# Optimization experiments

Hardware: AMD Instinct MI355X
Metric: run time of the kernel (lower is better)

## Reference

```python
import jax, jax.numpy as jnp
import numpy as np

B, D, INNER, OUT = 8192, 256, 64, 256


def setup_inputs() -> dict:
    key = jax.random.key(0)
    ks = jax.random.split(key, 10)
    s = 0.1
    return {
        "x": jax.random.normal(ks[0], (B, D), dtype=jnp.float32),
        # per-feature inner MLPs: Linear(1, inner) -> ReLU -> Linear(inner, 1)
        "w1": jax.random.normal(ks[1], (D, INNER), dtype=jnp.float32) * s,
        "b1": jax.random.normal(ks[2], (D, INNER), dtype=jnp.float32) * s,
        "w2": jax.random.normal(ks[3], (D, INNER), dtype=jnp.float32) * s,
        "b2": jax.random.normal(ks[4], (D,), dtype=jnp.float32) * s,
        # outer MLP: Linear(D, inner) -> ReLU -> Linear(inner, out)
        "wo1": jax.random.normal(ks[5], (INNER, D), dtype=jnp.float32) * s,
        "bo1": jax.random.normal(ks[6], (INNER,), dtype=jnp.float32) * s,
        "wo2": jax.random.normal(ks[7], (OUT, INNER), dtype=jnp.float32) * s,
        "bo2": jax.random.normal(ks[8], (OUT,), dtype=jnp.float32) * s,
    }


def reference(x, w1, b1, w2, b2, wo1, bo1, wo2, bo2):
    # Vectorized per-feature tiny MLPs: h[b,d,i] = relu(x[b,d]*w1[d,i] + b1[d,i])
    h = jax.nn.relu(x[:, :, None] * w1[None, :, :] + b1[None, :, :])  # [B, D, INNER]
    inner = jnp.einsum('bdi,di->bd', h, w2) + b2[None, :]             # [B, D]
    # Outer MLP
    g = jax.nn.relu(inner @ wo1.T + bo1)                              # [B, INNER]
    return g @ wo2.T + bo2                                            # [B, OUT]
```

## Files before the change

### kernel.cpp

```cpp
#include <hip/hip_runtime.h>
#include <hip/hip_bf16.h>


#define B_TOT 8192
#define D_DIM 256
#define I_DIM 64
#define O_DIM 256
#define RB 16
#define NT 512

typedef __hip_bfloat16 bf16;
using short8 = __attribute__((ext_vector_type(8))) short;
using f32x4  = __attribute__((ext_vector_type(4))) float;


__global__ __launch_bounds__(256)
void kal_prep(const float* __restrict__ w1, const float* __restrict__ b1,
              const float* __restrict__ w2, const float* __restrict__ wo1,
              const float* __restrict__ wo2, float4* __restrict__ ws) {
    int idx = blockIdx.x * 256 + threadIdx.x;
    if (idx < 16384) {
        int i = idx >> 8;
        int d = idx & 255;
        ws[idx] = make_float4(w1[d * I_DIM + i], b1[d * I_DIM + i],
                              w2[d * I_DIM + i], 0.0f);
    } else if (idx < 32768) {
        int r  = idx - 16384;
        int kc = r >> 11;
        int rem = r & 2047;
        int j  = rem >> 5;
        int kk = rem & 31;
        bf16* pbB = (bf16*)(ws + 16384);
        pbB[r] = __float2bfloat16(wo1[j * D_DIM + kc * 32 + kk]);
    } else if (idx < 49152) {
        int r  = idx - 32768;
        int kc = r >> 13;
        int rem = r & 8191;
        int o  = rem >> 5;
        int kk = rem & 31;
        bf16* pcB = (bf16*)(ws + 16384) + 16384;
        pcB[r] = __float2bfloat16(wo2[o * I_DIM + kc * 32 + kk]);
    }
}

__global__ __launch_bounds__(NT)
void kal_main(const float* __restrict__ x,  const float* __restrict__ b2,
              const float* __restrict__ bo1, const float* __restrict__ bo2,
              const float4* __restrict__ ws, float* __restrict__ out) {
    const float4* pa  = ws;
    const bf16*   pbB = (const bf16*)(ws + 16384);
    const bf16*   pcB = pbB + 16384;

    __shared__ bf16 inner_bf[RB][264];
    __shared__ bf16 g_bf[RB][72];

    const int t    = threadIdx.x;
    const int row0 = blockIdx.x * RB;

    {
        const int d    = t & 255;
        const int half = t >> 8;
        float xv[8], acc[8];
        const float b2v = b2[d];
        #pragma unroll
        for (int b = 0; b < 8; ++b) {
            xv[b]  = x[(row0 + half * 8 + b) * D_DIM + d];
            acc[b] = b2v;
        }
        #pragma unroll 4
        for (int i = 0; i < I_DIM; ++i) {
            const float4 w = pa[i * D_DIM + d];
            #pragma unroll
            for (int b = 0; b < 8; ++b) {
                float h = fmaf(xv[b], w.x, w.y);
                h = fmaxf(h, 0.0f);
                acc[b] = fmaf(h, w.z, acc[b]);
            }
        }
        #pragma unroll
        for (int b = 0; b < 8; ++b)
            inner_bf[half * 8 + b][d] = __float2bfloat16(acc[b]);
    }
    __syncthreads();

    const int lane = t & 63;
    const int wave = t >> 6;
    const int col  = lane & 15;
    const int quad = lane >> 4;

    if (wave < 4) {
        const int j0 = wave * 16;
        f32x4 acc = {0.f, 0.f, 0.f, 0.f};
        #pragma unroll
        for (int kc = 0; kc < 8; ++kc) {
            short8 af = *(const short8*)&inner_bf[col][kc * 32 + quad * 8];
            short8 bfr = *(const short8*)&pbB[(kc * 64 + j0 + col) * 32 + quad * 8];
            acc = __builtin_amdgcn_mfma_f32_16x16x32_bf16(af, bfr, acc, 0, 0, 0);
        }
        const float bo1v = bo1[j0 + col];
        #pragma unroll
        for (int r = 0; r < 4; ++r) {
            const int row = quad * 4 + r;
            g_bf[row][j0 + col] = __float2bfloat16(fmaxf(acc[r] + bo1v, 0.0f));
        }
    }
    __syncthreads();

    #pragma unroll
    for (int tile = 0; tile < 2; ++tile) {
        const int o0 = wave * 16 + tile * 128;
        f32x4 acc = {0.f, 0.f, 0.f, 0.f};
        #pragma unroll
        for (int kc = 0; kc < 2; ++kc) {
            short8 af = *(const short8*)&g_bf[col][kc * 32 + quad * 8];
            short8 bfr = *(const short8*)&pcB[(kc * 256 + o0 + col) * 32 + quad * 8];
            acc = __builtin_amdgcn_mfma_f32_16x16x32_bf16(af, bfr, acc, 0, 0, 0);
        }
        const float bo2v = bo2[o0 + col];
        #pragma unroll
        for (int r = 0; r < 4; ++r)
            out[(row0 + quad * 4 + r) * O_DIM + o0 + col] = acc[r] + bo2v;
    }
}

extern "C" void kernel_launch(void* const* d_in, const int* in_sizes, int n_in,
                              void* d_out, int out_size, void* d_ws, size_t ws_size,
                              hipStream_t stream) {
    const float* x   = (const float*)d_in[0];
    const float* w1  = (const float*)d_in[1];
    const float* b1  = (const float*)d_in[2];
    const float* w2  = (const float*)d_in[3];
    const float* b2  = (const float*)d_in[4];
    const float* wo1 = (const float*)d_in[5];
    const float* bo1 = (const float*)d_in[6];
    const float* wo2 = (const float*)d_in[7];
    const float* bo2 = (const float*)d_in[8];
    float* out = (float*)d_out;
    float4* ws = (float4*)d_ws;

    kal_prep<<<(49152 + 255) / 256, 256, 0, stream>>>(w1, b1, w2, wo1, wo2, ws);
    kal_main<<<B_TOT / RB, NT, 0, stream>>>(x, b2, bo1, bo2, ws, out);
}
```

Measured before the change: 91.39 us.

## Double rows per block and convert outer weights to bf16 inline

Each block now processes 32 rows with 1024 threads instead of 16 rows with 512, halving the grid and spreading more waves over the two MFMA GEMMs. The prep kernel no longer builds bf16 copies of wo1/wo2; the main kernel loads fp32 weights directly and converts them to bf16 fragments in registers. Inner-loop unrolling is raised from 4 to 8. This shrinks the prep kernel but adds per-block conversion work and reads fp32 weights twice as wide. The 1024-thread blocks may also lower occupancy.

```diff
diff --git a/kernel.cpp b/kernel.cpp
--- a/kernel.cpp
+++ b/kernel.cpp
@@ -6,8 +6,8 @@
 #define D_DIM 256
 #define I_DIM 64
 #define O_DIM 256
-#define RB 16
-#define NT 512
+#define RB 32
+#define NT 1024
 
 typedef __hip_bfloat16 bf16;
 using short8 = __attribute__((ext_vector_type(8))) short;
@@ -16,41 +16,31 @@
 
 __global__ __launch_bounds__(256)
 void kal_prep(const float* __restrict__ w1, const float* __restrict__ b1,
-              const float* __restrict__ w2, const float* __restrict__ wo1,
-              const float* __restrict__ wo2, float4* __restrict__ ws) {
+              const float* __restrict__ w2, float4* __restrict__ ws) {
     int idx = blockIdx.x * 256 + threadIdx.x;
-    if (idx < 16384) {
-        int i = idx >> 8;
-        int d = idx & 255;
-        ws[idx] = make_float4(w1[d * I_DIM + i], b1[d * I_DIM + i],
-                              w2[d * I_DIM + i], 0.0f);
-    } else if (idx < 32768) {
-        int r  = idx - 16384;
-        int kc = r >> 11;
-        int rem = r & 2047;
-        int j  = rem >> 5;
-        int kk = rem & 31;
-        bf16* pbB = (bf16*)(ws + 16384);
-        pbB[r] = __float2bfloat16(wo1[j * D_DIM + kc * 32 + kk]);
-    } else if (idx < 49152) {
-        int r  = idx - 32768;
-        int kc = r >> 13;
-        int rem = r & 8191;
-        int o  = rem >> 5;
-        int kk = rem & 31;
-        bf16* pcB = (bf16*)(ws + 16384) + 16384;
-        pcB[r] = __float2bfloat16(wo2[o * I_DIM + kc * 32 + kk]);
-    }
+    int i = idx >> 8;
+    int d = idx & 255;
+    ws[idx] = make_float4(w1[d * I_DIM + i], b1[d * I_DIM + i],
+                          w2[d * I_DIM + i], 0.0f);
+}
+
+static __device__ __forceinline__ short f2bs(float f) {
+    bf16 h = __float2bfloat16(f);
+    return *reinterpret_cast<short*>(&h);
+}
+
+static __device__ __forceinline__ short8 cvt_frag(float4 a, float4 b) {
+    short8 r;
+    r[0] = f2bs(a.x); r[1] = f2bs(a.y); r[2] = f2bs(a.z); r[3] = f2bs(a.w);
+    r[4] = f2bs(b.x); r[5] = f2bs(b.y); r[6] = f2bs(b.z); r[7] = f2bs(b.w);
+    return r;
 }
 
 __global__ __launch_bounds__(NT)
 void kal_main(const float* __restrict__ x,  const float* __restrict__ b2,
               const float* __restrict__ bo1, const float* __restrict__ bo2,
-              const float4* __restrict__ ws, float* __restrict__ out) {
-    const float4* pa  = ws;
-    const bf16*   pbB = (const bf16*)(ws + 16384);
-    const bf16*   pcB = pbB + 16384;
-
+              const float* __restrict__ wo1, const float* __restrict__ wo2,
+              const float4* __restrict__ pa, float* __restrict__ out) {
     __shared__ bf16 inner_bf[RB][264];
     __shared__ bf16 g_bf[RB][72];
 
@@ -58,16 +48,16 @@
     const int row0 = blockIdx.x * RB;
 
     {
-        const int d    = t & 255;
-        const int half = t >> 8;
+        const int d = t & 255;
+        const int q = t >> 8;
         float xv[8], acc[8];
         const float b2v = b2[d];
         #pragma unroll
         for (int b = 0; b < 8; ++b) {
-            xv[b]  = x[(row0 + half * 8 + b) * D_DIM + d];
+            xv[b]  = x[(row0 + q * 8 + b) * D_DIM + d];
             acc[b] = b2v;
         }
-        #pragma unroll 4
+        #pragma unroll 8
         for (int i = 0; i < I_DIM; ++i) {
             const float4 w = pa[i * D_DIM + d];
             #pragma unroll
@@ -79,7 +69,7 @@
         }
         #pragma unroll
         for (int b = 0; b < 8; ++b)
-            inner_bf[half * 8 + b][d] = __float2bfloat16(acc[b]);
+            inner_bf[q * 8 + b][d] = __float2bfloat16(acc[b]);
     }
     __syncthreads();
 
@@ -88,38 +78,47 @@
     const int col  = lane & 15;
     const int quad = lane >> 4;
 
-    if (wave < 4) {
-        const int j0 = wave * 16;
+    if (wave < 8) {
+        const int mt = wave >> 2;
+        const int j0 = (wave & 3) * 16;
+        const int jr = j0 + col;
         f32x4 acc = {0.f, 0.f, 0.f, 0.f};
         #pragma unroll
         for (int kc = 0; kc < 8; ++kc) {
-            short8 af = *(const short8*)&inner_bf[col][kc * 32 + quad * 8];
-            short8 bfr = *(const short8*)&pbB[(kc * 64 + j0 + col) * 32 + quad * 8];
+            short8 af = *(const short8*)&inner_bf[mt * 16 + col][kc * 32 + quad * 8];
+            const float4* wp = (const float4*)&wo1[jr * D_DIM + kc * 32 + quad * 8];
+            short8 bfr = cvt_frag(wp[0], wp[1]);
             acc = __builtin_amdgcn_mfma_f32_16x16x32_bf16(af, bfr, acc, 0, 0, 0);
         }
-        const float bo1v = bo1[j0 + col];
+        const float bo1v = bo1[jr];
         #pragma unroll
         for (int r = 0; r < 4; ++r) {
-            const int row = quad * 4 + r;
-            g_bf[row][j0 + col] = __float2bfloat16(fmaxf(acc[r] + bo1v, 0.0f));
+            const int row = mt * 16 + quad * 4 + r;
+            g_bf[row][jr] = __float2bfloat16(fmaxf(acc[r] + bo1v, 0.0f));
         }
     }
     __syncthreads();
 
-    #pragma unroll
-    for (int tile = 0; tile < 2; ++tile) {
-        const int o0 = wave * 16 + tile * 128;
-        f32x4 acc = {0.f, 0.f, 0.f, 0.f};
+    {
+        const int mt = wave >> 3;
+        const int jw = wave & 7;
         #pragma unroll
-        for (int kc = 0; kc < 2; ++kc) {
-            short8 af = *(const short8*)&g_bf[col][kc * 32 + quad * 8];
-            short8 bfr = *(const short8*)&pcB[(kc * 256 + o0 + col) * 32 + quad * 8];
-            acc = __builtin_amdgcn_mfma_f32_16x16x32_bf16(af, bfr, acc, 0, 0, 0);
+        for (int tt = 0; tt < 2; ++tt) {
+            const int o0 = (jw * 2 + tt) * 16;
+            const int oc = o0 + col;
+            f32x4 acc = {0.f, 0.f, 0.f, 0.f};
+            #pragma unroll
+            for (int kc = 0; kc < 2; ++kc) {
+                short8 af = *(const short8*)&g_bf[mt * 16 + col][kc * 32 + quad * 8];
+                const float4* wp = (const float4*)&wo2[oc * I_DIM + kc * 32 + quad * 8];
+                short8 bfr = cvt_frag(wp[0], wp[1]);
+                acc = __builtin_amdgcn_mfma_f32_16x16x32_bf16(af, bfr, acc, 0, 0, 0);
+            }
+            const float bo2v = bo2[oc];
+            #pragma unroll
+            for (int r = 0; r < 4; ++r)
+                out[(row0 + mt * 16 + quad * 4 + r) * O_DIM + oc] = acc[r] + bo2v;
         }
-        const float bo2v = bo2[o0 + col];
-        #pragma unroll
-        for (int r = 0; r < 4; ++r)
-            out[(row0 + quad * 4 + r) * O_DIM + o0 + col] = acc[r] + bo2v;
     }
 }
 
@@ -138,6 +137,6 @@
     float* out = (float*)d_out;
     float4* ws = (float4*)d_ws;
 
-    kal_prep<<<(49152 + 255) / 256, 256, 0, stream>>>(w1, b1, w2, wo1, wo2, ws);
-    kal_main<<<B_TOT / RB, NT, 0, stream>>>(x, b2, bo1, bo2, ws, out);
+    kal_prep<<<64, 256, 0, stream>>>(w1, b1, w2, ws);
+    kal_main<<<B_TOT / RB, NT, 0, stream>>>(x, b2, bo1, bo2, wo1, wo2, ws, out);
 }
```

New measurement: 95.41 us. 4.4% more time.

## Use packed fp16 math with fdot2 for per-feature inner MLPs

Applied to the files above, without the earlier changes.

The per-feature inner MLP stage moves from fp32 FMAs to packed half2 FMA and max, with v_dot2 accumulating into fp32. The prep kernel repacks w1, b1 and w2 into fp16 triplets, so the weight stream shrinks from 16-byte float4 entries to 6 bytes per inner unit. This targets the VALU-bound inner loop, roughly halving instruction count, and cuts the weight bandwidth. In exchange, x, the weights and the hidden activations lose precision in fp16.

```diff
diff --git a/kernel.cpp b/kernel.cpp
--- a/kernel.cpp
+++ b/kernel.cpp
@@ -12,33 +12,57 @@
 typedef __hip_bfloat16 bf16;
 using short8 = __attribute__((ext_vector_type(8))) short;
 using f32x4  = __attribute__((ext_vector_type(4))) float;
+using hlf2   = __attribute__((ext_vector_type(2))) _Float16;
 
+
+static __device__ __forceinline__ unsigned h2bits(float a, float b) {
+    hlf2 v = { (_Float16)a, (_Float16)b };
+    return __builtin_bit_cast(unsigned, v);
+}
+static __device__ __forceinline__ hlf2 bch2(unsigned u) {
+    return __builtin_bit_cast(hlf2, u);
+}
 
 __global__ __launch_bounds__(256)
 void kal_prep(const float* __restrict__ w1, const float* __restrict__ b1,
               const float* __restrict__ w2, const float* __restrict__ wo1,
-              const float* __restrict__ wo2, float4* __restrict__ ws) {
+              const float* __restrict__ wo2, uint4* __restrict__ ws) {
     int idx = blockIdx.x * 256 + threadIdx.x;
-    if (idx < 16384) {
-        int i = idx >> 8;
+    if (idx < 2048) {
+        int g = idx >> 8;
         int d = idx & 255;
-        ws[idx] = make_float4(w1[d * I_DIM + i], b1[d * I_DIM + i],
-                              w2[d * I_DIM + i], 0.0f);
-    } else if (idx < 32768) {
-        int r  = idx - 16384;
+        float v1[8], vb[8], v2[8];
+        #pragma unroll
+        for (int k = 0; k < 8; ++k) {
+            v1[k] = w1[d * I_DIM + g * 8 + k];
+            vb[k] = b1[d * I_DIM + g * 8 + k];
+            v2[k] = w2[d * I_DIM + g * 8 + k];
+        }
+        unsigned w1p[4], b1p[4], w2p[4];
+        #pragma unroll
+        for (int k = 0; k < 4; ++k) {
+            w1p[k] = h2bits(v1[2*k], v1[2*k+1]);
+            b1p[k] = h2bits(vb[2*k], vb[2*k+1]);
+            w2p[k] = h2bits(v2[2*k], v2[2*k+1]);
+        }
+        ws[(g*3+0)*256 + d] = make_uint4(w1p[0], b1p[0], w2p[0], w1p[1]);
+        ws[(g*3+1)*256 + d] = make_uint4(b1p[1], w2p[1], w1p[2], b1p[2]);
+        ws[(g*3+2)*256 + d] = make_uint4(w2p[2], w1p[3], b1p[3], w2p[3]);
+    } else if (idx < 18432) {
+        int r  = idx - 2048;
         int kc = r >> 11;
         int rem = r & 2047;
         int j  = rem >> 5;
         int kk = rem & 31;
-        bf16* pbB = (bf16*)(ws + 16384);
+        bf16* pbB = (bf16*)((char*)ws + 98304);
         pbB[r] = __float2bfloat16(wo1[j * D_DIM + kc * 32 + kk]);
-    } else if (idx < 49152) {
-        int r  = idx - 32768;
+    } else {
+        int r  = idx - 18432;
         int kc = r >> 13;
         int rem = r & 8191;
         int o  = rem >> 5;
         int kk = rem & 31;
-        bf16* pcB = (bf16*)(ws + 16384) + 16384;
+        bf16* pcB = (bf16*)((char*)ws + 131072);
         pcB[r] = __float2bfloat16(wo2[o * I_DIM + kc * 32 + kk]);
     }
 }
@@ -46,10 +70,10 @@
 __global__ __launch_bounds__(NT)
 void kal_main(const float* __restrict__ x,  const float* __restrict__ b2,
               const float* __restrict__ bo1, const float* __restrict__ bo2,
-              const float4* __restrict__ ws, float* __restrict__ out) {
-    const float4* pa  = ws;
-    const bf16*   pbB = (const bf16*)(ws + 16384);
-    const bf16*   pcB = pbB + 16384;
+              const uint4* __restrict__ ws, float* __restrict__ out) {
+    const uint4* paq = ws;
+    const bf16*  pbB = (const bf16*)((const char*)ws + 98304);
+    const bf16*  pcB = (const bf16*)((const char*)ws + 131072);
 
     __shared__ bf16 inner_bf[RB][264];
     __shared__ bf16 g_bf[RB][72];
@@ -60,21 +84,34 @@
     {
         const int d    = t & 255;
         const int half = t >> 8;
-        float xv[8], acc[8];
+        hlf2  xh[8];
+        float acc[8];
         const float b2v = b2[d];
         #pragma unroll
         for (int b = 0; b < 8; ++b) {
-            xv[b]  = x[(row0 + half * 8 + b) * D_DIM + d];
+            float xv = x[(row0 + half * 8 + b) * D_DIM + d];
+            _Float16 xf = (_Float16)xv;
+            xh[b]  = (hlf2){ xf, xf };
             acc[b] = b2v;
         }
-        #pragma unroll 4
-        for (int i = 0; i < I_DIM; ++i) {
-            const float4 w = pa[i * D_DIM + d];
+        const uint4* pw = paq + d;
+        const hlf2 hz = { (_Float16)0.0f, (_Float16)0.0f };
+        #pragma unroll 2
+        for (int g = 0; g < 8; ++g) {
+            const uint4 q0 = pw[(g*3 + 0) * 256];
+            const uint4 q1 = pw[(g*3 + 1) * 256];
+            const uint4 q2 = pw[(g*3 + 2) * 256];
+            const hlf2 w1p[4] = { bch2(q0.x), bch2(q0.w), bch2(q1.z), bch2(q2.y) };
+            const hlf2 b1p[4] = { bch2(q0.y), bch2(q1.x), bch2(q1.w), bch2(q2.z) };
+            const hlf2 w2p[4] = { bch2(q0.z), bch2(q1.y), bch2(q2.x), bch2(q2.w) };
             #pragma unroll
-            for (int b = 0; b < 8; ++b) {
-                float h = fmaf(xv[b], w.x, w.y);
-                h = fmaxf(h, 0.0f);
-                acc[b] = fmaf(h, w.z, acc[b]);
+            for (int k = 0; k < 4; ++k) {
+                #pragma unroll
+                for (int b = 0; b < 8; ++b) {
+                    hlf2 h = __builtin_elementwise_fma(xh[b], w1p[k], b1p[k]);
+                    h = __builtin_elementwise_max(h, hz);
+                    acc[b] = __builtin_amdgcn_fdot2(h, w2p[k], acc[b], false);
+                }
             }
         }
         #pragma unroll
@@ -136,8 +173,8 @@
     const float* wo2 = (const float*)d_in[7];
     const float* bo2 = (const float*)d_in[8];
     float* out = (float*)d_out;
-    float4* ws = (float4*)d_ws;
+    uint4* ws = (uint4*)d_ws;
 
-    kal_prep<<<(49152 + 255) / 256, 256, 0, stream>>>(w1, b1, w2, wo1, wo2, ws);
+    kal_prep<<<136, 256, 0, stream>>>(w1, b1, w2, wo1, wo2, ws);
     kal_main<<<B_TOT / RB, NT, 0, stream>>>(x, b2, bo1, bo2, ws, out);
 }
```

New measurement: 86.16 us. -5.7%, faster.
